# Optimization experiments

Hardware: AMD Instinct MI355X
Metric: run time of the kernel (lower is better)

Reference implementation:

```python
import jax, jax.numpy as jnp
import numpy as np

IDIM = 1024
ODIM = 1024
NHEADS = 16
B, S = 4, 1024


def setup_inputs() -> dict:
    key = jax.random.key(0)
    k1, k2, k3, k4, k5, k6 = jax.random.split(key, 6)
    m_feats = jax.random.normal(k1, (B, S, IDIM), dtype=jnp.float32)
    mask = jax.random.randint(k2, (B, S), 0, 2, dtype=jnp.int32)
    # torch Linear weights stored pre-transposed: y = x @ W + b
    W_c = jax.random.normal(k3, (IDIM, 2 * ODIM), dtype=jnp.float32) * 0.02
    b_c = jnp.zeros((2 * ODIM,), dtype=jnp.float32)
    W_v = jax.random.normal(k4, (IDIM, ODIM), dtype=jnp.float32) * 0.02
    b_v = jnp.zeros((ODIM,), dtype=jnp.float32)
    return {"m_feats": m_feats, "mask": mask, "W_c": W_c, "b_c": b_c, "W_v": W_v, "b_v": b_v}


def reference(m_feats, mask, W_c, b_c, W_v, b_v):
    # dp = 0.0 -> dropout is identity (eval-mode equivalence)
    Bn, Sn, _ = m_feats.shape
    odim = W_v.shape[1]
    dh = odim // NHEADS
    m_k = m_feats @ W_v + b_v            # v_lin  -> keys   [B,S,odim]
    m_trans = m_feats @ W_c + b_c        # c_lin  -> [B,S,2*odim]
    m_q = m_trans[..., :odim]            # queries
    m_v = m_trans[..., odim:]            # values
    mk = m_k.reshape(Bn, Sn, NHEADS, dh)
    mq = m_q.reshape(Bn, Sn, NHEADS, dh)
    mv = m_v.reshape(Bn, Sn, NHEADS, dh)
    # original: scores = K @ Q^T / sqrt(dh); softmax over the Q (last) axis
    scores = jnp.einsum('bihd,bjhd->bhij', mk, mq) / jnp.sqrt(jnp.float32(dh))
    maskf = mask.astype(jnp.float32)
    scores = jnp.where(maskf[:, None, None, :] == 0.0, jnp.float32(-1e9), scores)
    w = jax.nn.softmax(scores, axis=-1)               # [B,H,S,S]
    r = jnp.einsum('bhij,bjhd->bihd', w, mv).reshape(Bn, Sn, odim)
    updated_m = m_feats + r
    return updated_m, w
```

## Files before the change

### kernel.cpp

```cpp
#include <hip/hip_runtime.h>
#include <cstddef>

typedef short short8 __attribute__((ext_vector_type(8)));
typedef float f32x4 __attribute__((ext_vector_type(4)));

#define SS 1024
#define NH 16
#define DH 64
#define NB 4

static __device__ __forceinline__ unsigned short f2bf(float f) {
    union { float f; unsigned int i; } x; x.f = f;
    unsigned int r = x.i + 0x7FFFu + ((x.i >> 16) & 1u);
    return (unsigned short)(r >> 16);
}
static __device__ __forceinline__ float bf2f(unsigned short u) {
    union { unsigned int i; float f; } x; x.i = ((unsigned int)u) << 16;
    return x.f;
}

static __device__ __forceinline__ void g2l16(const void* g, void* l) {
    __builtin_amdgcn_global_load_lds(
        (const __attribute__((address_space(1))) unsigned int*)g,
        (__attribute__((address_space(3))) unsigned int*)l, 16, 0, 0);
}

__global__ __launch_bounds__(256) void prep(const float* __restrict__ mf,
                                            unsigned short* __restrict__ mfb,
                                            const float* __restrict__ Wv,
                                            const float* __restrict__ Wc,
                                            unsigned short* __restrict__ WT) {
    __shared__ float tile[32][33];
    int bx = blockIdx.x;
    int t = threadIdx.x;
    if (bx < 2048) {
        size_t i = ((size_t)bx * 256 + t) * 8;
        float4 v0 = *(const float4*)(mf + i);
        float4 v1 = *(const float4*)(mf + i + 4);
        short8 o;
        o[0] = (short)f2bf(v0.x); o[1] = (short)f2bf(v0.y);
        o[2] = (short)f2bf(v0.z); o[3] = (short)f2bf(v0.w);
        o[4] = (short)f2bf(v1.x); o[5] = (short)f2bf(v1.y);
        o[6] = (short)f2bf(v1.z); o[7] = (short)f2bf(v1.w);
        *(short8*)(mfb + i) = o;
        return;
    }
    bx -= 2048;
    int n0 = (bx % 96) * 32, k0 = (bx / 96) * 32;
    int kr = t >> 3, nc = (t & 7) * 4;
    const float* src; int ld; int nn = n0 + nc;
    if (n0 < 1024) { src = Wv; ld = 1024; } else { src = Wc; ld = 2048; nn -= 1024; }
    float4 v = *(const float4*)(src + (size_t)(k0 + kr) * ld + nn);
    tile[kr][nc + 0] = v.x; tile[kr][nc + 1] = v.y;
    tile[kr][nc + 2] = v.z; tile[kr][nc + 3] = v.w;
    __syncthreads();
    int nr = t >> 3, kc = (t & 7) * 4;
    short4 o;
    o.x = (short)f2bf(tile[kc + 0][nr]); o.y = (short)f2bf(tile[kc + 1][nr]);
    o.z = (short)f2bf(tile[kc + 2][nr]); o.w = (short)f2bf(tile[kc + 3][nr]);
    *(short4*)(WT + (size_t)(n0 + nr) * 1024 + k0 + kc) = o;
}

__global__ __launch_bounds__(256) void gemm_kqv(const unsigned short* __restrict__ A,
                                                const unsigned short* __restrict__ BT,
                                                const float* __restrict__ bv,
                                                const float* __restrict__ bc,
                                                unsigned short* __restrict__ kq,
                                                unsigned short* __restrict__ mvT) {
    __shared__ __align__(16) unsigned short As[2][128 * 32];
    __shared__ __align__(16) unsigned short Bs[2][128 * 32];
    int lin = blockIdx.y * 24 + blockIdx.x;
    int xcd = lin & 7, idx = lin >> 3;
    int cx = xcd & 1, cy = xcd >> 1;
    int xi = idx % 12, yi = idx / 12;
    int n0 = (cx * 12 + xi) * 128;
    int m0 = (cy * 8 + yi) * 128;

    int tid = threadIdx.x, lane = tid & 63, wv = tid >> 6;
    int wm = wv >> 1, wn = wv & 1;
    int lq = lane & 15, quad = lane >> 4;

    f32x4 zero = {0.f, 0.f, 0.f, 0.f};
    f32x4 acc[4][4];
#pragma unroll
    for (int i = 0; i < 4; ++i)
#pragma unroll
        for (int j = 0; j < 4; ++j) acc[i][j] = zero;

    int r0 = tid >> 2, s0 = tid & 3;
    int c0 = s0 ^ ((r0 >> 1) & 3);
    int r1 = (tid + 256) >> 2, s1 = tid & 3;
    int c1 = s1 ^ ((r1 >> 1) & 3);

    const unsigned short* Abase0 = A + (size_t)(m0 + r0) * 1024 + c0 * 8;
    const unsigned short* Abase1 = A + (size_t)(m0 + r1) * 1024 + c1 * 8;
    const unsigned short* Bbase0 = BT + (size_t)(n0 + r0) * 1024 + c0 * 8;
    const unsigned short* Bbase1 = BT + (size_t)(n0 + r1) * 1024 + c1 * 8;

    g2l16(Abase0, As[0] + tid * 8);
    g2l16(Abase1, As[0] + (tid + 256) * 8);
    g2l16(Bbase0, Bs[0] + tid * 8);
    g2l16(Bbase1, Bs[0] + (tid + 256) * 8);
    __syncthreads();

#pragma unroll 2
    for (int t32 = 0; t32 < 32; ++t32) {
        int cur = t32 & 1;
        if (t32 < 31) {
            int nkt = (t32 + 1) * 32;
            g2l16(Abase0 + nkt, As[cur ^ 1] + tid * 8);
            g2l16(Abase1 + nkt, As[cur ^ 1] + (tid + 256) * 8);
            g2l16(Bbase0 + nkt, Bs[cur ^ 1] + tid * 8);
            g2l16(Bbase1 + nkt, Bs[cur ^ 1] + (tid + 256) * 8);
        }

        short8 af[4], bfr[4];
#pragma unroll
        for (int i = 0; i < 4; ++i) {
            int Ra = wm * 64 + i * 16 + lq;
            af[i] = *(const short8*)(As[cur] + Ra * 32 + (quad ^ ((Ra >> 1) & 3)) * 8);
            int Rb = wn * 64 + i * 16 + lq;
            bfr[i] = *(const short8*)(Bs[cur] + Rb * 32 + (quad ^ ((Rb >> 1) & 3)) * 8);
        }
#pragma unroll
        for (int mi = 0; mi < 4; ++mi)
#pragma unroll
            for (int ni = 0; ni < 4; ++ni)
                acc[mi][ni] = __builtin_amdgcn_mfma_f32_16x16x32_bf16(af[mi], bfr[ni], acc[mi][ni], 0, 0, 0);

        __syncthreads();
    }

#pragma unroll
    for (int mi = 0; mi < 4; ++mi) {
#pragma unroll
        for (int ni = 0; ni < 4; ++ni) {
            int colg = n0 + wn * 64 + ni * 16 + lq;
            float bias = (colg < 1024) ? bv[colg] : bc[colg - 1024];
            if (colg < 2048) {
#pragma unroll
                for (int r = 0; r < 4; ++r) {
                    int rowg = m0 + wm * 64 + mi * 16 + quad * 4 + r;
                    kq[(size_t)rowg * 2048 + colg] = f2bf(acc[mi][ni][r] + bias);
                }
            } else {
                int c = colg - 2048;
                int hh = c >> 6, dd = c & 63;
#pragma unroll
                for (int r = 0; r < 4; ++r) {
                    int rowg = m0 + wm * 64 + mi * 16 + quad * 4 + r;
                    int bb = rowg >> 10, jj = rowg & 1023;
                    mvT[((size_t)(bb * NH + hh) * DH + dd) * 1024 + jj] =
                        f2bf(acc[mi][ni][r] + bias);
                }
            }
        }
    }
}

__global__ __launch_bounds__(512, 1) void attn_kernel(const unsigned short* __restrict__ kq,
                                                      const unsigned short* __restrict__ mvT,
                                                      const int* __restrict__ mask,
                                                      const float* __restrict__ m_feats,
                                                      float* __restrict__ out0,
                                                      float* __restrict__ out1) {
    __shared__ __align__(16) unsigned short mk_s[64 * 72];
    __shared__ __align__(16) unsigned short s_exp[64 * 1032];
    __shared__ float wsum[8][64];
    __shared__ float inv_s[64];

    int tid = threadIdx.x;
    int lane = tid & 63, wv = tid >> 6;
    int lq = lane & 15, quad = lane >> 4;

    int blk = ((int)blockIdx.x & 7) * 128 + ((int)blockIdx.x >> 3);
    int it = blk & 15;
    int bh = blk >> 4;
    int h = bh & (NH - 1), b = bh >> 4;
    int i0 = it * 64;

    const float SC = 0.18033688011112042f;
    const unsigned short* mqb = kq + (size_t)b * SS * 2048 + 1024 + h * 64 + quad * 8;
    const int* maskb = mask + (size_t)b * SS;

    short8 qb[2][4][2];
    int qm[2][4];
    float sums[4][4] = {{0.f,0.f,0.f,0.f},{0.f,0.f,0.f,0.f},{0.f,0.f,0.f,0.f},{0.f,0.f,0.f,0.f}};

#define QLOAD(p, s)                                                          \
    {                                                                        \
        int jb_ = (s) * 512 + wv * 64;                                       \
        _Pragma("unroll") for (int js = 0; js < 4; ++js) {                   \
            int jg_ = jb_ + js * 16 + lq;                                    \
            size_t ro_ = (size_t)jg_ * 2048;                                 \
            qb[p][js][0] = *(const short8*)(mqb + ro_);                      \
            qb[p][js][1] = *(const short8*)(mqb + ro_ + 32);                 \
            qm[p][js] = maskb[jg_];                                          \
        }                                                                    \
    }

#define QCOMP(p, s)                                                          \
    {                                                                        \
        int jb_ = (s) * 512 + wv * 64;                                       \
        _Pragma("unroll") for (int js = 0; js < 4; ++js) {                   \
            int jc_ = jb_ + js * 16 + lq;                                    \
            _Pragma("unroll") for (int ti = 0; ti < 4; ++ti) {               \
                f32x4 acc = {0.f, 0.f, 0.f, 0.f};                            \
                acc = __builtin_amdgcn_mfma_f32_16x16x32_bf16(a[ti][0], qb[p][js][0], acc, 0, 0, 0); \
                acc = __builtin_amdgcn_mfma_f32_16x16x32_bf16(a[ti][1], qb[p][js][1], acc, 0, 0, 0); \
                _Pragma("unroll") for (int r = 0; r < 4; ++r) {              \
                    float e = qm[p][js] ? __builtin_amdgcn_exp2f(acc[r] * SC) : 0.f; \
                    sums[ti][r] += e;                                        \
                    s_exp[(ti * 16 + quad * 4 + r) * 1032 + jc_] = f2bf(e);  \
                }                                                            \
            }                                                                \
        }                                                                    \
    }

    QLOAD(0, 0);

    int wq = wv & 3, tp = wv >> 2;
    float mf8[2][4];
#pragma unroll
    for (int tt = 0; tt < 2; ++tt)
#pragma unroll
        for (int r = 0; r < 4; ++r) {
            size_t o = (size_t)(b * SS + i0 + (tp * 2 + tt) * 16 + quad * 4 + r) * 1024
                       + h * 64 + wq * 16 + lq;
            mf8[tt][r] = m_feats[o];
        }

    {
        int row = tid >> 3, ch = tid & 7;
        int4 v = *(const int4*)(kq + (size_t)(b * SS + i0 + row) * 2048 + h * 64 + ch * 8);
        *(int4*)(mk_s + row * 72 + ch * 8) = v;
    }
    QLOAD(1, 1);
    __syncthreads();

    short8 a[4][2];
#pragma unroll
    for (int ti = 0; ti < 4; ++ti) {
        a[ti][0] = *(const short8*)(mk_s + (ti * 16 + lq) * 72 + 0 * 32 + quad * 8);
        a[ti][1] = *(const short8*)(mk_s + (ti * 16 + lq) * 72 + 1 * 32 + quad * 8);
    }

    QCOMP(0, 0);
    QCOMP(1, 1);
#undef QLOAD
#undef QCOMP

    f32x4 racc[2] = {{0.f, 0.f, 0.f, 0.f}, {0.f, 0.f, 0.f, 0.f}};
    const unsigned short* mvb = mvT + ((size_t)bh * DH + wq * 16 + lq) * 1024 + quad * 8;
    size_t wbase = ((size_t)bh * SS + i0) * SS;
    short8 vbuf[4][4];

#define VLOAD(p, ko)                                                         \
    {                                                                        \
        _Pragma("unroll") for (int k2 = 0; k2 < 4; ++k2)                     \
            vbuf[p][k2] = *(const short8*)(mvb + ((ko) * 4 + k2) * 32);      \
    }

#define VCOMP(p, ko)                                                         \
    {                                                                        \
        _Pragma("unroll") for (int k2 = 0; k2 < 4; ++k2) {                   \
            _Pragma("unroll") for (int tt = 0; tt < 2; ++tt) {               \
                short8 ae = *(const short8*)(s_exp + ((tp * 2 + tt) * 16 + lq) * 1032 + ((ko) * 4 + k2) * 32 + quad * 8); \
                racc[tt] = __builtin_amdgcn_mfma_f32_16x16x32_bf16(ae, vbuf[p][k2], racc[tt], 0, 0, 0); \
            }                                                                \
        }                                                                    \
    }

#define WOUT(pr)                                                             \
    {                                                                        \
        int row_ = (pr) * 2 + (tid >> 8);                                    \
        float iv = inv_s[row_];                                              \
        short4 ev = *(const short4*)(s_exp + row_ * 1032 + (tid & 255) * 4); \
        f32x4 wo;                                                            \
        wo[0] = bf2f((unsigned short)ev.x) * iv;                             \
        wo[1] = bf2f((unsigned short)ev.y) * iv;                             \
        wo[2] = bf2f((unsigned short)ev.z) * iv;                             \
        wo[3] = bf2f((unsigned short)ev.w) * iv;                             \
        __builtin_nontemporal_store(wo, (f32x4*)(out1 + wbase + (size_t)row_ * SS + (tid & 255) * 4)); \
    }

    VLOAD(0, 0); VLOAD(1, 1);

#pragma unroll
    for (int ti = 0; ti < 4; ++ti)
#pragma unroll
        for (int r = 0; r < 4; ++r) {
            float s = sums[ti][r];
            s += __shfl_xor(s, 1); s += __shfl_xor(s, 2);
            s += __shfl_xor(s, 4); s += __shfl_xor(s, 8);
            if (lq == 0) wsum[wv][ti * 16 + quad * 4 + r] = s;
        }
    __syncthreads();
    if (tid < 64) {
        float s = wsum[0][tid] + wsum[1][tid] + wsum[2][tid] + wsum[3][tid]
                + wsum[4][tid] + wsum[5][tid] + wsum[6][tid] + wsum[7][tid];
        inv_s[tid] = 1.0f / s;
    }
    VLOAD(2, 2); VLOAD(3, 3);
    __syncthreads();

    VCOMP(0, 0); VLOAD(0, 4); WOUT(0);  WOUT(1);  WOUT(2);  WOUT(3);
    VCOMP(1, 1); VLOAD(1, 5); WOUT(4);  WOUT(5);  WOUT(6);  WOUT(7);
    VCOMP(2, 2); VLOAD(2, 6); WOUT(8);  WOUT(9);  WOUT(10); WOUT(11);
    VCOMP(3, 3); VLOAD(3, 7); WOUT(12); WOUT(13); WOUT(14); WOUT(15);
    VCOMP(0, 4); WOUT(16); WOUT(17); WOUT(18); WOUT(19);
    VCOMP(1, 5); WOUT(20); WOUT(21); WOUT(22); WOUT(23);
    VCOMP(2, 6); WOUT(24); WOUT(25); WOUT(26); WOUT(27);
    VCOMP(3, 7); WOUT(28); WOUT(29); WOUT(30); WOUT(31);
#undef VLOAD
#undef VCOMP
#undef WOUT

#pragma unroll
    for (int tt = 0; tt < 2; ++tt)
#pragma unroll
        for (int r = 0; r < 4; ++r) {
            int row = (tp * 2 + tt) * 16 + quad * 4 + r;
            size_t o = (size_t)(b * SS + i0 + row) * 1024 + h * 64 + wq * 16 + lq;
            __builtin_nontemporal_store(mf8[tt][r] + racc[tt][r] * inv_s[row], out0 + o);
        }
}

extern "C" void kernel_launch(void* const* d_in, const int* in_sizes, int n_in,
                              void* d_out, int out_size, void* d_ws, size_t ws_size,
                              hipStream_t stream) {
    const float* m_feats = (const float*)d_in[0];
    const int*   mask    = (const int*)d_in[1];
    const float* W_c     = (const float*)d_in[2];
    const float* b_c     = (const float*)d_in[3];
    const float* W_v     = (const float*)d_in[4];
    const float* b_v     = (const float*)d_in[5];

    float* out0 = (float*)d_out;
    float* out1 = out0 + (size_t)NB * SS * 1024;

    unsigned short* mf_bf = (unsigned short*)d_ws;
    unsigned short* WT    = mf_bf + (size_t)4096 * 1024;
    unsigned short* kq    = WT + (size_t)3072 * 1024;
    unsigned short* mvT   = kq + (size_t)4096 * 2048;

    prep<<<dim3(5120), dim3(256), 0, stream>>>(m_feats, mf_bf, W_v, W_c, WT);
    gemm_kqv<<<dim3(24, 32), dim3(256), 0, stream>>>(mf_bf, WT, b_v, b_c, kq, mvT);
    attn_kernel<<<dim3(1024), dim3(512), 0, stream>>>(kq, mvT, mask, m_feats, out0, out1);
}
```

Before: 399.4 us.

## Halve attention query tile to 32 rows and raise occupancy to four blocks

```diff
diff --git a/kernel.cpp b/kernel.cpp
--- a/kernel.cpp
+++ b/kernel.cpp
@@ -158,26 +158,27 @@
     }
 }
 
-__global__ __launch_bounds__(512, 1) void attn_kernel(const unsigned short* __restrict__ kq,
+__global__ __launch_bounds__(512, 4) void attn_kernel(const unsigned short* __restrict__ kq,
                                                       const unsigned short* __restrict__ mvT,
                                                       const int* __restrict__ mask,
                                                       const float* __restrict__ m_feats,
                                                       float* __restrict__ out0,
                                                       float* __restrict__ out1) {
-    __shared__ __align__(16) unsigned short mk_s[64 * 72];
-    __shared__ __align__(16) unsigned short s_exp[64 * 1032];
-    __shared__ float wsum[8][64];
-    __shared__ float inv_s[64];
+    __shared__ __align__(16) unsigned short mk_s[32 * 72];
+    __shared__ __align__(16) unsigned short s_exp[32 * 1032];
+    __shared__ float wsum[8][32];
+    __shared__ float inv_s[32];
 
     int tid = threadIdx.x;
     int lane = tid & 63, wv = tid >> 6;
     int lq = lane & 15, quad = lane >> 4;
-
-    int blk = ((int)blockIdx.x & 7) * 128 + ((int)blockIdx.x >> 3);
-    int it = blk & 15;
-    int bh = blk >> 4;
+    int wq = wv & 3, tp = wv >> 2;
+
+    int blk = ((int)blockIdx.x & 7) * 256 + ((int)blockIdx.x >> 3);
+    int it = blk & 31;
+    int bh = blk >> 5;
     int h = bh & (NH - 1), b = bh >> 4;
-    int i0 = it * 64;
+    int i0 = it * 32;
 
     const float SC = 0.18033688011112042f;
     const unsigned short* mqb = kq + (size_t)b * SS * 2048 + 1024 + h * 64 + quad * 8;
@@ -185,7 +186,7 @@
 
     short8 qb[2][4][2];
     int qm[2][4];
-    float sums[4][4] = {{0.f,0.f,0.f,0.f},{0.f,0.f,0.f,0.f},{0.f,0.f,0.f,0.f},{0.f,0.f,0.f,0.f}};
+    float sums[2][4] = {{0.f, 0.f, 0.f, 0.f}, {0.f, 0.f, 0.f, 0.f}};
 
 #define QLOAD(p, s)                                                          \
     {                                                                        \
@@ -204,7 +205,7 @@
         int jb_ = (s) * 512 + wv * 64;                                       \
         _Pragma("unroll") for (int js = 0; js < 4; ++js) {                   \
             int jc_ = jb_ + js * 16 + lq;                                    \
-            _Pragma("unroll") for (int ti = 0; ti < 4; ++ti) {               \
+            _Pragma("unroll") for (int ti = 0; ti < 2; ++ti) {               \
                 f32x4 acc = {0.f, 0.f, 0.f, 0.f};                            \
                 acc = __builtin_amdgcn_mfma_f32_16x16x32_bf16(a[ti][0], qb[p][js][0], acc, 0, 0, 0); \
                 acc = __builtin_amdgcn_mfma_f32_16x16x32_bf16(a[ti][1], qb[p][js][1], acc, 0, 0, 0); \
@@ -219,18 +220,15 @@
 
     QLOAD(0, 0);
 
-    int wq = wv & 3, tp = wv >> 2;
-    float mf8[2][4];
-#pragma unroll
-    for (int tt = 0; tt < 2; ++tt)
-#pragma unroll
-        for (int r = 0; r < 4; ++r) {
-            size_t o = (size_t)(b * SS + i0 + (tp * 2 + tt) * 16 + quad * 4 + r) * 1024
-                       + h * 64 + wq * 16 + lq;
-            mf8[tt][r] = m_feats[o];
-        }
-
-    {
+    float mf4[4];
+#pragma unroll
+    for (int r = 0; r < 4; ++r) {
+        size_t o = (size_t)(b * SS + i0 + tp * 16 + quad * 4 + r) * 1024
+                   + h * 64 + wq * 16 + lq;
+        mf4[r] = m_feats[o];
+    }
+
+    if (tid < 256) {
         int row = tid >> 3, ch = tid & 7;
         int4 v = *(const int4*)(kq + (size_t)(b * SS + i0 + row) * 2048 + h * 64 + ch * 8);
         *(int4*)(mk_s + row * 72 + ch * 8) = v;
@@ -238,9 +236,9 @@
     QLOAD(1, 1);
     __syncthreads();
 
-    short8 a[4][2];
-#pragma unroll
-    for (int ti = 0; ti < 4; ++ti) {
+    short8 a[2][2];
+#pragma unroll
+    for (int ti = 0; ti < 2; ++ti) {
         a[ti][0] = *(const short8*)(mk_s + (ti * 16 + lq) * 72 + 0 * 32 + quad * 8);
         a[ti][1] = *(const short8*)(mk_s + (ti * 16 + lq) * 72 + 1 * 32 + quad * 8);
     }
@@ -250,7 +248,7 @@
 #undef QLOAD
 #undef QCOMP
 
-    f32x4 racc[2] = {{0.f, 0.f, 0.f, 0.f}, {0.f, 0.f, 0.f, 0.f}};
+    f32x4 racc = {0.f, 0.f, 0.f, 0.f};
     const unsigned short* mvb = mvT + ((size_t)bh * DH + wq * 16 + lq) * 1024 + quad * 8;
     size_t wbase = ((size_t)bh * SS + i0) * SS;
     short8 vbuf[4][4];
@@ -264,10 +262,8 @@
 #define VCOMP(p, ko)                                                         \
     {                                                                        \
         _Pragma("unroll") for (int k2 = 0; k2 < 4; ++k2) {                   \
-            _Pragma("unroll") for (int tt = 0; tt < 2; ++tt) {               \
-                short8 ae = *(const short8*)(s_exp + ((tp * 2 + tt) * 16 + lq) * 1032 + ((ko) * 4 + k2) * 32 + quad * 8); \
-                racc[tt] = __builtin_amdgcn_mfma_f32_16x16x32_bf16(ae, vbuf[p][k2], racc[tt], 0, 0, 0); \
-            }                                                                \
+            short8 ae = *(const short8*)(s_exp + (tp * 16 + lq) * 1032 + ((ko) * 4 + k2) * 32 + quad * 8); \
+            racc = __builtin_amdgcn_mfma_f32_16x16x32_bf16(ae, vbuf[p][k2], racc, 0, 0, 0); \
         }                                                                    \
     }
 
@@ -287,7 +283,7 @@
     VLOAD(0, 0); VLOAD(1, 1);
 
 #pragma unroll
-    for (int ti = 0; ti < 4; ++ti)
+    for (int ti = 0; ti < 2; ++ti)
 #pragma unroll
         for (int r = 0; r < 4; ++r) {
             float s = sums[ti][r];
@@ -296,7 +292,7 @@
             if (lq == 0) wsum[wv][ti * 16 + quad * 4 + r] = s;
         }
     __syncthreads();
-    if (tid < 64) {
+    if (tid < 32) {
         float s = wsum[0][tid] + wsum[1][tid] + wsum[2][tid] + wsum[3][tid]
                 + wsum[4][tid] + wsum[5][tid] + wsum[6][tid] + wsum[7][tid];
         inv_s[tid] = 1.0f / s;
@@ -304,26 +300,24 @@
     VLOAD(2, 2); VLOAD(3, 3);
     __syncthreads();
 
-    VCOMP(0, 0); VLOAD(0, 4); WOUT(0);  WOUT(1);  WOUT(2);  WOUT(3);
-    VCOMP(1, 1); VLOAD(1, 5); WOUT(4);  WOUT(5);  WOUT(6);  WOUT(7);
-    VCOMP(2, 2); VLOAD(2, 6); WOUT(8);  WOUT(9);  WOUT(10); WOUT(11);
-    VCOMP(3, 3); VLOAD(3, 7); WOUT(12); WOUT(13); WOUT(14); WOUT(15);
-    VCOMP(0, 4); WOUT(16); WOUT(17); WOUT(18); WOUT(19);
-    VCOMP(1, 5); WOUT(20); WOUT(21); WOUT(22); WOUT(23);
-    VCOMP(2, 6); WOUT(24); WOUT(25); WOUT(26); WOUT(27);
-    VCOMP(3, 7); WOUT(28); WOUT(29); WOUT(30); WOUT(31);
+    VCOMP(0, 0); VLOAD(0, 4); WOUT(0);  WOUT(1);
+    VCOMP(1, 1); VLOAD(1, 5); WOUT(2);  WOUT(3);
+    VCOMP(2, 2); VLOAD(2, 6); WOUT(4);  WOUT(5);
+    VCOMP(3, 3); VLOAD(3, 7); WOUT(6);  WOUT(7);
+    VCOMP(0, 4); WOUT(8);  WOUT(9);
+    VCOMP(1, 5); WOUT(10); WOUT(11);
+    VCOMP(2, 6); WOUT(12); WOUT(13);
+    VCOMP(3, 7); WOUT(14); WOUT(15);
 #undef VLOAD
 #undef VCOMP
 #undef WOUT
 
 #pragma unroll
-    for (int tt = 0; tt < 2; ++tt)
-#pragma unroll
-        for (int r = 0; r < 4; ++r) {
-            int row = (tp * 2 + tt) * 16 + quad * 4 + r;
-            size_t o = (size_t)(b * SS + i0 + row) * 1024 + h * 64 + wq * 16 + lq;
-            __builtin_nontemporal_store(mf8[tt][r] + racc[tt][r] * inv_s[row], out0 + o);
-        }
+    for (int r = 0; r < 4; ++r) {
+        int row = tp * 16 + quad * 4 + r;
+        size_t o = (size_t)(b * SS + i0 + row) * 1024 + h * 64 + wq * 16 + lq;
+        __builtin_nontemporal_store(mf4[r] + racc[r] * inv_s[row], out0 + o);
+    }
 }
 
 extern "C" void kernel_launch(void* const* d_in, const int* in_sizes, int n_in,
@@ -346,5 +340,5 @@
 
     prep<<<dim3(5120), dim3(256), 0, stream>>>(m_feats, mf_bf, W_v, W_c, WT);
     gemm_kqv<<<dim3(24, 32), dim3(256), 0, stream>>>(mf_bf, WT, b_v, b_c, kq, mvT);
-    attn_kernel<<<dim3(1024), dim3(512), 0, stream>>>(kq, mvT, mask, m_feats, out0, out1);
-}
+    attn_kernel<<<dim3(2048), dim3(512), 0, stream>>>(kq, mvT, mask, m_feats, out0, out1);
+}
```

Result: no change. 399.8 us (+0.1%).
